# Performance work log

Measured on AMD Instinct MI355X. Metric: run time of the kernel, lower is better.

## Reference

```python
import jax, jax.numpy as jnp
import numpy as np

D_MODEL = 1024
NUM_HEADS = 16
D_K = D_MODEL // NUM_HEADS
B, S = 2, 2048


def setup_inputs() -> dict:
    key = jax.random.key(0)
    ks = jax.random.split(key, 6)
    scale = 1.0 / np.sqrt(D_MODEL)
    x = jax.random.normal(ks[0], (B, S, D_MODEL), dtype=jnp.float32)
    # causal mask: 1 where masked (future positions), per masked_fill(mask == 1, -inf)
    mask = jnp.triu(jnp.ones((S, S), dtype=jnp.int32), k=1)
    Wq = jax.random.normal(ks[1], (D_MODEL, D_MODEL), dtype=jnp.float32) * scale
    Wk = jax.random.normal(ks[2], (D_MODEL, D_MODEL), dtype=jnp.float32) * scale
    Wv = jax.random.normal(ks[3], (D_MODEL, D_MODEL), dtype=jnp.float32) * scale
    Wo = jax.random.normal(ks[4], (D_MODEL, D_MODEL), dtype=jnp.float32) * scale
    zeros = jnp.zeros((D_MODEL,), dtype=jnp.float32)
    return {"x": x, "mask": mask, "Wq": Wq, "bq": zeros, "Wk": Wk, "bk": zeros,
            "Wv": Wv, "bv": zeros, "Wo": Wo, "bo": zeros}


def reference(x, mask, Wq, bq, Wk, bk, Wv, bv, Wo, bo):
    b, s, d = x.shape
    # linear projections (torch nn.Linear: x @ W^T + b; here W stored as [in, out])
    Q = x @ Wq + bq
    K = x @ Wk + bk
    V = x @ Wv + bv
    # split heads -> (b, h, s, d_k)
    def split(t):
        return t.reshape(b, s, NUM_HEADS, D_K).transpose(0, 2, 1, 3)
    Q, K, V = split(Q), split(K), split(V)
    scale = 1.0 / jnp.sqrt(jnp.float32(D_K))
    scores = jnp.einsum("bhqd,bhkd->bhqk", Q, K) * scale  # (b,h,s,s)
    scores = jnp.where(mask[None, None, :, :] == 1, -jnp.inf, scores)
    attn = jax.nn.softmax(scores, axis=-1)
    out = jnp.einsum("bhqk,bhkd->bhqd", attn, V)
    out = out.transpose(0, 2, 1, 3).reshape(b, s, d)  # concat heads
    return out @ Wo + bo
```

## Files before the change

### kernel.cpp

```cpp
#include <hip/hip_runtime.h>
#include <hip/hip_bf16.h>
#include <cstdint>
#include <cmath>

#define DM 1024
#define NH 16
#define DK 64
#define NB 2
#define SS 2048
#define MM (NB*SS)

typedef unsigned short u16;
typedef uint32_t u32;
typedef __attribute__((ext_vector_type(4))) float f32x4;
typedef __attribute__((ext_vector_type(8))) short s16x8;
typedef __attribute__((ext_vector_type(2))) uint32_t u32x2;

__device__ __forceinline__ u16 f2bf(float f) {
    __hip_bfloat16 h = __float2bfloat16(f);
    return __builtin_bit_cast(u16, h);
}
__device__ __forceinline__ float bf2f(u16 u) {
    u32 x = (u32)u << 16;
    return __builtin_bit_cast(float, x);
}

__device__ __forceinline__ u32 cvtpk(float a, float b) {
    u32 r;
    asm("v_cvt_pk_bf16_f32 %0, %1, %2" : "=v"(r) : "v"(a), "v"(b));
    return r;
}

__device__ __forceinline__ void gload_lds16(void* lds, const void* g) {
    __builtin_amdgcn_global_load_lds(
        (const __attribute__((address_space(1))) uint32_t*)g,
        (__attribute__((address_space(3))) uint32_t*)lds, 16, 0, 0);
}

__device__ __forceinline__ int swz(int row, int cb) {
    return row * 128 + ((((cb) >> 4) ^ (row & 7)) << 4) + ((cb) & 15);
}

__global__ void mha_prep(const float* __restrict__ x, u16* __restrict__ xb,
                         const float* __restrict__ W0, const float* __restrict__ W1,
                         const float* __restrict__ W2, const float* __restrict__ W3,
                         u16* __restrict__ WtBase) {
    const int bid = blockIdx.x, tid = threadIdx.x;
    if (bid < 4096) {
        int i = (bid * 256 + tid) * 4;
        float4 v = *reinterpret_cast<const float4*>(x + i);
        ushort4 o;
        o.x = f2bf(v.x); o.y = f2bf(v.y); o.z = f2bf(v.z); o.w = f2bf(v.w);
        *reinterpret_cast<ushort4*>(xb + i) = o;
        return;
    }
    __shared__ float t[32][33];
    const int b2 = bid - 4096;
    const int mat = b2 >> 10, rem = b2 & 1023;
    const int cx = rem & 31, cy = rem >> 5;
    const float* W = (mat == 0) ? W0 : (mat == 1) ? W1 : (mat == 2) ? W2 : W3;
    u16* Wt = WtBase + (size_t)mat * DM * DM;
    const int c0 = cx * 32, r0 = cy * 32;
    const int tx = tid & 31, ty = tid >> 5;
#pragma unroll
    for (int i = ty; i < 32; i += 8)
        t[i][tx] = W[(size_t)(r0 + i) * DM + c0 + tx];
    __syncthreads();
#pragma unroll
    for (int i = ty; i < 32; i += 8)
        Wt[(size_t)(c0 + i) * DM + r0 + tx] = f2bf(t[tx][i]);
}

__device__ __forceinline__ void gemm_loop_db(const u16* __restrict__ A, const u16* __restrict__ Bt,
                                             int m0, int n0, char* smem , f32x4 acc[4][4]) {
    const int tid = threadIdx.x;
    const int wave = tid >> 6, lane = tid & 63;
    const int lr = lane & 15, kg = lane >> 4;
    const int wr = wave >> 1, wc = wave & 1;

    auto STAGE = [&](int buf, int k0) {
        char* As = smem + buf * 32768;
        char* Bs = As + 16384;
#pragma unroll
        for (int i = 0; i < 4; ++i) {
            const int o   = ((wave * 4 + i) * 64 + lane) * 16;
            const int row = o >> 7;
            const int kb  = o & 127;
            gload_lds16(As + o, A  + (size_t)(m0 + row) * DM + k0 + (kb >> 1));
            gload_lds16(Bs + o, Bt + (size_t)(n0 + row) * DM + k0 + (kb >> 1));
        }
    };

    STAGE(0, 0);
    for (int t = 0; t < 16; ++t) {
        if (t + 1 < 16) {
            STAGE((t + 1) & 1, (t + 1) * 64);
            asm volatile("s_waitcnt vmcnt(8)" ::: "memory");
        } else {
            asm volatile("s_waitcnt vmcnt(0)" ::: "memory");
        }
        __builtin_amdgcn_sched_barrier(0);
        __builtin_amdgcn_s_barrier();
        __builtin_amdgcn_sched_barrier(0);

        const u16 (*As)[64] = reinterpret_cast<const u16(*)[64]>(smem + (t & 1) * 32768);
        const u16 (*Bs)[64] = reinterpret_cast<const u16(*)[64]>(smem + (t & 1) * 32768 + 16384);
#pragma unroll
        for (int kk = 0; kk < 64; kk += 32) {
            s16x8 a[4], b[4];
#pragma unroll
            for (int m = 0; m < 4; ++m)
                a[m] = *reinterpret_cast<const s16x8*>(&As[wr * 64 + m * 16 + lr][kk + kg * 8]);
#pragma unroll
            for (int n = 0; n < 4; ++n)
                b[n] = *reinterpret_cast<const s16x8*>(&Bs[wc * 64 + n * 16 + lr][kk + kg * 8]);
#pragma unroll
            for (int m = 0; m < 4; ++m)
#pragma unroll
                for (int n = 0; n < 4; ++n)
                    acc[m][n] = __builtin_amdgcn_mfma_f32_16x16x32_bf16(a[m], b[n], acc[m][n], 0, 0, 0);
        }
        __builtin_amdgcn_sched_barrier(0);
        __builtin_amdgcn_s_barrier();
        __builtin_amdgcn_sched_barrier(0);
    }
}

__global__ __launch_bounds__(256, 2) void mha_gemm_qkv(const u16* __restrict__ xb, const u16* __restrict__ Wt,
                                                       const float* __restrict__ bq, const float* __restrict__ bk,
                                                       const float* __restrict__ bv, u16* __restrict__ qkv) {
    __shared__ __align__(16) char smem[65536];
    const int m0 = blockIdx.x * 128, n0 = blockIdx.y * 128;
    const int z = blockIdx.z;
    const float* bias = (z == 0) ? bq : (z == 1) ? bk : bv;
    const float scale = (z == 0) ? 0.125f * 1.44269504088896f : 1.0f;
    u16* Cout = qkv + (size_t)z * MM * DM;

    f32x4 acc[4][4] = {};
    gemm_loop_db(xb, Wt + (size_t)z * DM * DM, m0, n0, smem, acc);

    const int tid = threadIdx.x;
    const int wave = tid >> 6, lane = tid & 63;
    const int lr = lane & 15, kg = lane >> 4;
    const int wr = wave >> 1, wc = wave & 1;

#pragma unroll
    for (int m = 0; m < 4; ++m)
#pragma unroll
        for (int n = 0; n < 4; ++n) {
            const int col = wc * 64 + n * 16 + lr;
            const float bv2 = bias[n0 + col];
#pragma unroll
            for (int j2 = 0; j2 < 4; ++j2) {
                const int row = wr * 64 + m * 16 + kg * 4 + j2;
                const float v = (acc[m][n][j2] + bv2) * scale;
                int imgoff;
                if (z == 0) {
                    imgoff = row * 256 + (col >> 6) * 128 + (col & 63) * 2;
                } else if (z == 1) {
                    imgoff = ((row >> 6) * 2 + (col >> 6)) * 8192 + swz(row & 63, (col & 63) * 2);
                } else {
                    imgoff = ((row >> 6) * 2 + (col >> 6)) * 8192
                           + swz(col & 63, ((row & 63) >> 1) * 4 + (row & 1) * 2);
                }
                *reinterpret_cast<u16*>(smem + imgoff) = f2bf(v);
            }
        }
    __syncthreads();
    const int bb = m0 >> 11, s0 = m0 & (SS - 1);
    const int kt0 = s0 >> 6, h0 = n0 >> 6;
#pragma unroll
    for (int it = 0; it < 8; ++it) {
        const int c = it * 256 + tid;
        const s16x8 v = *reinterpret_cast<const s16x8*>(smem + c * 16);
        u16* dst;
        if (z == 0) {
            const int srow = c >> 4, inrow = c & 15;
            const int hl = inrow >> 3, d0 = (inrow & 7) * 8;
            dst = Cout + (((size_t)(bb * NH + h0 + hl) * SS + (s0 + srow)) * DK) + d0;
        } else {
            const int quad = c >> 9, off = (c & 511) * 8;
            const int ktl = quad >> 1, hl = quad & 1;
            dst = Cout + ((size_t)(bb * NH + h0 + hl) * 32 + kt0 + ktl) * 4096 + off;
        }
        *reinterpret_cast<s16x8*>(dst) = v;
    }
}

__global__ __launch_bounds__(256, 2) void mha_gemm_out(const u16* __restrict__ AO, const u16* __restrict__ WoT,
                                                       const float* __restrict__ bo, float* __restrict__ out) {
    __shared__ __align__(16) char smem[65536];
    const int m0 = blockIdx.x * 128, n0 = blockIdx.y * 128;

    f32x4 acc[4][4] = {};
    gemm_loop_db(AO, WoT, m0, n0, smem, acc);

    const int tid = threadIdx.x;
    const int wave = tid >> 6, lane = tid & 63;
    const int lr = lane & 15, kg = lane >> 4;
    const int wr = wave >> 1, wc = wave & 1;
#pragma unroll
    for (int m = 0; m < 4; ++m)
#pragma unroll
        for (int n = 0; n < 4; ++n) {
            const int col = n0 + wc * 64 + n * 16 + lr;
            const float bv = bo[col];
#pragma unroll
            for (int j2 = 0; j2 < 4; ++j2) {
                const int row = m0 + wr * 64 + m * 16 + kg * 4 + j2;
                out[(size_t)row * DM + col] = acc[m][n][j2] + bv;
            }
        }
}

__device__ const unsigned char JQT[48] = {
    15,31,30,31, 14,29,30,28,29, 13,27,28,26,27, 12,25,26,24,25,
    11,23,24,22,23, 10,21,22,20,21, 9,19,20,18,19, 8,17,18,16,17,
    7,16, 6,5,4,3,2,1,0};
__device__ const unsigned char JKS[48] = {
    0,0,15,16, 0,0,0,14,15, 0,0,0,13,14, 0,0,0,12,13,
    0,0,0,11,12, 0,0,0,10,11, 0,0,0,9,10, 0,0,0,8,9,
    0,0, 0,0,0,0,0,0,0};
__device__ const unsigned char JKL[48] = {
    16,16,16,16, 15,15,15,15,15, 14,14,14,14,14, 13,13,13,13,13,
    12,12,12,12,12, 11,11,11,11,11, 10,10,10,10,10, 9,9,9,9,9,
    8,8, 7,6,5,4,3,2,1};
__device__ const unsigned char JSL[48] = {
    255,30,29,31, 255,26,28,25,27, 255,22,24,21,23, 255,18,20,17,19,
    255,14,16,13,15, 255,10,12,9,11, 255,6,8,5,7, 255,2,4,1,3,
    255,0, 255,255,255,255,255,255,255};

__global__ __launch_bounds__(256, 4) void mha_attn(const u16* __restrict__ Qb, const u16* __restrict__ Kswz,
                                                   const u16* __restrict__ Vtswz, u16* __restrict__ AO,
                                                   u16* __restrict__ Opart, float* __restrict__ lpart) {
    __shared__ __align__(16) char lds[40960];

    const int bid = blockIdx.x;
    const int bh  = bid & 31;
    const int job = bid >> 5;
    const int qt   = JQT[job];
    const int kst  = JKS[job];
    const int klen = JKL[job];
    const int slot = JSL[job];
    const int qb = qt * 64;

    const int tid = threadIdx.x, w = tid >> 6, lane = tid & 63;
    const int lr = lane & 15, kg = lane >> 4;

    const u16* Qh = Qb + (size_t)bh * SS * DK;
    const char* Ktiles = (const char*)(Kswz  + (size_t)bh * 32 * 4096);
    const char* Vtiles = (const char*)(Vtswz + (size_t)bh * 32 * 4096);
    const int bb = bh >> 4, hh = bh & (NH - 1);
    char* psb = lds + 32768 + w * 2048;
    const int o = tid * 16;

    const int qrow = qb + w * 16 + lr;
    const s16x8 qf0 = *reinterpret_cast<const s16x8*>(Qh + (size_t)qrow * DK + kg * 8);
    const s16x8 qf1 = *reinterpret_cast<const s16x8*>(Qh + (size_t)qrow * DK + 32 + kg * 8);
    f32x4 accO[4] = {};
    float lp = 0.f;

    const int kend = kst + klen;
    {
        const char* Kt = Ktiles + kst * 8192;
        const char* Vt = Vtiles + kst * 8192;
        gload_lds16(lds + o,                 Kt + o);
        gload_lds16(lds + o + 4096,          Kt + o + 4096);
        gload_lds16(lds + 16384 + o,         Vt + o);
        gload_lds16(lds + 16384 + o + 4096,  Vt + o + 4096);
    }

    for (int t = kst; t < kend; ++t) {
        const int buf = (t - kst) & 1;
        asm volatile("s_waitcnt vmcnt(0)" ::: "memory");
        __syncthreads();
        if (t + 1 < kend) {
            const char* Kt = Ktiles + (t + 1) * 8192;
            const char* Vt = Vtiles + (t + 1) * 8192;
            char* kb2 = lds + (buf ^ 1) * 8192;
            char* vb2 = lds + 16384 + (buf ^ 1) * 8192;
            gload_lds16(kb2 + o,        Kt + o);
            gload_lds16(kb2 + o + 4096, Kt + o + 4096);
            gload_lds16(vb2 + o,        Vt + o);
            gload_lds16(vb2 + o + 4096, Vt + o + 4096);
        }
        const char* ksb = lds + buf * 8192;
        const char* vtb = lds + 16384 + buf * 8192;

        f32x4 sc[4];
#pragma unroll
        for (int f = 0; f < 4; ++f) {
            s16x8 kf0 = *reinterpret_cast<const s16x8*>(ksb + swz(f * 16 + lr, kg * 16));
            s16x8 kf1 = *reinterpret_cast<const s16x8*>(ksb + swz(f * 16 + lr, 64 + kg * 16));
            f32x4 s = {};
            s = __builtin_amdgcn_mfma_f32_16x16x32_bf16(kf0, qf0, s, 0, 0, 0);
            s = __builtin_amdgcn_mfma_f32_16x16x32_bf16(kf1, qf1, s, 0, 0, 0);
            sc[f] = s;
        }
#pragma unroll
        for (int f = 0; f < 4; ++f)
#pragma unroll
            for (int j = 0; j < 4; ++j)
                sc[f][j] = __builtin_amdgcn_exp2f(sc[f][j]);
        if (t == qt) {
            const int qloc = w * 16 + lr;
#pragma unroll
            for (int f = 0; f < 4; ++f) {
                const int kc = f * 16 + kg * 4;
#pragma unroll
                for (int j = 0; j < 4; ++j)
                    if (kc + j > qloc) sc[f][j] = 0.f;
            }
        }
        float fs0 = 0.f, fs1 = 0.f;
#pragma unroll
        for (int f = 0; f < 4; ++f) {
            u32x2 pp;
            pp[0] = cvtpk(sc[f][0], sc[f][1]);
            pp[1] = cvtpk(sc[f][2], sc[f][3]);
            *reinterpret_cast<u32x2*>(psb + swz(lr, f * 32 + kg * 8)) = pp;
            const float s01 = sc[f][0] + sc[f][1], s23 = sc[f][2] + sc[f][3];
            if (f & 1) fs1 += s01 + s23; else fs0 += s01 + s23;
        }
        lp += fs0 + fs1;

        const s16x8 pf0 = *reinterpret_cast<const s16x8*>(psb + swz(lr, kg * 16));
        const s16x8 pf1 = *reinterpret_cast<const s16x8*>(psb + swz(lr, 64 + kg * 16));
#pragma unroll
        for (int db = 0; db < 4; ++db) {
            s16x8 vf0 = *reinterpret_cast<const s16x8*>(vtb + swz(db * 16 + lr, kg * 16));
            s16x8 vf1 = *reinterpret_cast<const s16x8*>(vtb + swz(db * 16 + lr, 64 + kg * 16));
            accO[db] = __builtin_amdgcn_mfma_f32_16x16x32_bf16(pf0, vf0, accO[db], 0, 0, 0);
            accO[db] = __builtin_amdgcn_mfma_f32_16x16x32_bf16(pf1, vf1, accO[db], 0, 0, 0);
        }
    }

    lp += __shfl_xor(lp, 16, 64);
    lp += __shfl_xor(lp, 32, 64);

    if (slot == 255) {
        float inv[4];
#pragma unroll
        for (int j = 0; j < 4; ++j)
            inv[j] = 1.0f / __shfl(lp, kg * 4 + j, 64);
#pragma unroll
        for (int db = 0; db < 4; ++db) {
            const int d = db * 16 + lr;
#pragma unroll
            for (int j = 0; j < 4; ++j) {
                const int s = qb + w * 16 + kg * 4 + j;
                AO[((size_t)(bb * SS + s)) * DM + hh * DK + d] = f2bf(accO[db][j] * inv[j]);
            }
        }
    } else {
        const int idx = bh * 32 + slot;
        u16* Od = Opart + (size_t)idx * 4096;
#pragma unroll
        for (int db = 0; db < 4; ++db) {
            const int d = db * 16 + lr;
#pragma unroll
            for (int j = 0; j < 4; ++j)
                Od[(w * 16 + kg * 4 + j) * 64 + d] = f2bf(accO[db][j]);
        }
        if (lane < 16)
            lpart[idx * 64 + w * 16 + lane] = lp;
    }
}

__global__ __launch_bounds__(256) void mha_combine(const u16* __restrict__ Opart,
                                                   const float* __restrict__ lpart,
                                                   u16* __restrict__ AO) {
    const int blk = blockIdx.x;
    const int bh = blk & 31, q = blk >> 5;
    const int qt = 16 + q;
    const int t = threadIdx.x;
    const int row = t >> 2, c0 = (t & 3) * 16;
    const int idx0 = bh * 32 + q * 2;
    const u16* O0 = Opart + (size_t)idx0 * 4096 + row * 64 + c0;
    const u16* O1 = O0 + 4096;
    const float l = lpart[idx0 * 64 + row] + lpart[(idx0 + 1) * 64 + row];
    const float inv = 1.0f / l;
    const int bb = bh >> 4, hh = bh & (NH - 1);
    const int s = qt * 64 + row;
    u16* dst = AO + ((size_t)(bb * SS + s)) * DM + hh * DK + c0;
#pragma unroll
    for (int h = 0; h < 2; ++h) {
        s16x8 a = *reinterpret_cast<const s16x8*>(O0 + h * 8);
        s16x8 b = *reinterpret_cast<const s16x8*>(O1 + h * 8);
        u16* ap = (u16*)&a; u16* bp = (u16*)&b;
        u16 ov[8];
#pragma unroll
        for (int i = 0; i < 8; ++i)
            ov[i] = f2bf((bf2f(ap[i]) + bf2f(bp[i])) * inv);
        *reinterpret_cast<ushort4*>(dst + h * 8) = *reinterpret_cast<ushort4*>(&ov[0]);
        *reinterpret_cast<ushort4*>(dst + h * 8 + 4) = *reinterpret_cast<ushort4*>(&ov[4]);
    }
}

extern "C" void kernel_launch(void* const* d_in, const int* in_sizes, int n_in,
                              void* d_out, int out_size, void* d_ws, size_t ws_size,
                              hipStream_t stream) {
    const float* x  = (const float*)d_in[0];
    const float* Wq = (const float*)d_in[2];
    const float* bq = (const float*)d_in[3];
    const float* Wk = (const float*)d_in[4];
    const float* bk = (const float*)d_in[5];
    const float* Wv = (const float*)d_in[6];
    const float* bv = (const float*)d_in[7];
    const float* Wo = (const float*)d_in[8];
    const float* bo = (const float*)d_in[9];
    float* out = (float*)d_out;

    char* ws = (char*)d_ws;
    u16* xb  = (u16*)(ws);
    u16* Wt  = (u16*)(ws + ((size_t)8  << 20));
    u16* qkv = (u16*)(ws + ((size_t)16 << 20));
    u16* AO  = (u16*)(ws + ((size_t)40 << 20));
    u16*   Opart = (u16*)(ws);
    float* lpart = (float*)(ws + ((size_t)8 << 20));

    mha_prep<<<dim3(8192), dim3(256), 0, stream>>>(x, xb, Wq, Wk, Wv, Wo, Wt);
    mha_gemm_qkv<<<dim3(32, 8, 3), dim3(256), 0, stream>>>(xb, Wt, bq, bk, bv, qkv);
    mha_attn<<<dim3(1536), dim3(256), 0, stream>>>(qkv, qkv + (size_t)4194304, qkv + (size_t)8388608,
                                                   AO, Opart, lpart);
    mha_combine<<<dim3(512), dim3(256), 0, stream>>>(Opart, lpart, AO);
    mha_gemm_out<<<dim3(32, 8), dim3(256), 0, stream>>>(AO, Wt + (size_t)3 * DM * DM, bo, out);
}
```

Baseline: 107.3 us.

## Rewrite QKV projection GEMM with 256x256 tiles, 8 waves, and phased prefetch

Replaces the 128x128, 4-wave QKV GEMM with a 256x256 tile computed by 8 waves (512 threads). The K loop is split into four quadrant phases, each issuing the next half-tile prefetch into a swizzled LDS double buffer ahead of its MFMAs, and MFMA blocks run at raised wave priority. The goal is more operand reuse per byte loaded and better overlap of loads with compute. The grid shrinks to 192 blocks, under one wave of blocks on a 256-CU part. The epilogue now writes scattered 2-byte global stores instead of staging through LDS for 16-byte coalesced writes, which may cost store bandwidth.

```diff
diff --git a/kernel.cpp b/kernel.cpp
--- a/kernel.cpp
+++ b/kernel.cpp
@@ -40,6 +40,10 @@
 __device__ __forceinline__ int swz(int row, int cb) {
     return row * 128 + ((((cb) >> 4) ^ (row & 7)) << 4) + ((cb) & 15);
 }
+
+#define FENCE_BAR  do { __builtin_amdgcn_sched_barrier(0); \
+                        __builtin_amdgcn_s_barrier();      \
+                        __builtin_amdgcn_sched_barrier(0); } while (0)
 
 __global__ void mha_prep(const float* __restrict__ x, u16* __restrict__ xb,
                          const float* __restrict__ W0, const float* __restrict__ W1,
@@ -71,6 +75,120 @@
         Wt[(size_t)(c0 + i) * DM + r0 + tx] = f2bf(t[tx][i]);
 }
 
+template<int QA, int QB>
+__device__ __forceinline__ void phase8(const char* smem, int cur,
+                                       int wm, int wn, int lr, int kg,
+                                       f32x4 (&acc)[8][4]) {
+    const char* Ab = smem + cur * 32768 + QA * 16384;
+    const char* Bb = smem + 65536 + cur * 32768 + QB * 16384;
+    s16x8 af[4][2], bf[2][2];
+#pragma unroll
+    for (int m = 0; m < 4; ++m)
+#pragma unroll
+        for (int ks = 0; ks < 2; ++ks)
+            af[m][ks] = *reinterpret_cast<const s16x8*>(Ab + swz(wm * 64 + m * 16 + lr, ks * 64 + kg * 16));
+#pragma unroll
+    for (int n = 0; n < 2; ++n)
+#pragma unroll
+        for (int ks = 0; ks < 2; ++ks)
+            bf[n][ks] = *reinterpret_cast<const s16x8*>(Bb + swz(wn * 32 + n * 16 + lr, ks * 64 + kg * 16));
+    __builtin_amdgcn_s_setprio(1);
+#pragma unroll
+    for (int m = 0; m < 4; ++m)
+#pragma unroll
+        for (int n = 0; n < 2; ++n)
+#pragma unroll
+            for (int ks = 0; ks < 2; ++ks)
+                acc[QA * 4 + m][QB * 2 + n] =
+                    __builtin_amdgcn_mfma_f32_16x16x32_bf16(af[m][ks], bf[n][ks],
+                                                            acc[QA * 4 + m][QB * 2 + n], 0, 0, 0);
+    __builtin_amdgcn_s_setprio(0);
+}
+
+__global__ __launch_bounds__(512, 2) void mha_gemm_qkv(const u16* __restrict__ xb, const u16* __restrict__ Wt,
+                                                       const float* __restrict__ bq, const float* __restrict__ bk,
+                                                       const float* __restrict__ bv, u16* __restrict__ qkv) {
+    __shared__ __align__(16) char smem[131072];
+    const int bid = blockIdx.x;
+    const int mtile = bid & 15, ntile = bid >> 4;
+    const int m0 = mtile * 256, n0g = ntile * 256;
+    const int z = n0g >> 10;
+    const int n0loc = n0g & 1023;
+    const u16* At  = xb + (size_t)m0 * DM;
+    const u16* Btm = Wt + (size_t)z * DM * DM + (size_t)n0loc * DM;
+    const float* bias = (z == 0) ? bq : (z == 1) ? bk : bv;
+    const float scale = (z == 0) ? 0.125f * 1.44269504088896f : 1.0f;
+    u16* Cout = qkv + (size_t)z * MM * DM;
+
+    const int tid = threadIdx.x, lane = tid & 63, wid = tid >> 6;
+    const int lr = lane & 15, kg = lane >> 4;
+    const int wm = wid >> 2, wn = wid & 3;
+    f32x4 acc[8][4] = {};
+
+    auto STAGE = [&](int isB, int half, int buf, int kt) {
+        char* base = smem + (isB ? 65536 : 0) + buf * 32768 + half * 16384;
+        const u16* src = isB ? Btm : At;
+#pragma unroll
+        for (int i = 0; i < 2; ++i) {
+            const int o = tid * 16 + i * 8192;
+            const int r = o >> 7, slot = (o >> 4) & 7;
+            gload_lds16(base + o,
+                        src + (size_t)(half * 128 + r) * DM + kt * 64 + ((slot ^ (r & 7)) << 3));
+        }
+    };
+
+    STAGE(0, 0, 0, 0); STAGE(1, 0, 0, 0); STAGE(0, 1, 0, 0); STAGE(1, 1, 0, 0);
+
+    for (int t = 0; t < 16; ++t) {
+        const int cur = t & 1, nxt = cur ^ 1;
+        const bool pf = (t + 1 < 16);
+        asm volatile("s_waitcnt vmcnt(4)" ::: "memory");
+        FENCE_BAR;
+        if (pf) STAGE(0, 0, nxt, t + 1);
+        phase8<0, 0>(smem, cur, wm, wn, lr, kg, acc);
+        if (pf) asm volatile("s_waitcnt vmcnt(4)" ::: "memory");
+        else    asm volatile("s_waitcnt vmcnt(2)" ::: "memory");
+        FENCE_BAR;
+        if (pf) STAGE(1, 0, nxt, t + 1);
+        phase8<1, 0>(smem, cur, wm, wn, lr, kg, acc);
+        if (pf) asm volatile("s_waitcnt vmcnt(4)" ::: "memory");
+        else    asm volatile("s_waitcnt vmcnt(0)" ::: "memory");
+        FENCE_BAR;
+        if (pf) STAGE(0, 1, nxt, t + 1);
+        phase8<1, 1>(smem, cur, wm, wn, lr, kg, acc);
+        if (pf) STAGE(1, 1, nxt, t + 1);
+        phase8<0, 1>(smem, cur, wm, wn, lr, kg, acc);
+    }
+
+#pragma unroll
+    for (int qa = 0; qa < 2; ++qa)
+#pragma unroll
+        for (int m = 0; m < 4; ++m)
+#pragma unroll
+            for (int qb = 0; qb < 2; ++qb)
+#pragma unroll
+                for (int n = 0; n < 2; ++n) {
+                    const int colg = n0loc + qb * 128 + wn * 32 + n * 16 + lr;
+                    const int h = colg >> 6, d = colg & 63;
+                    const float bv2 = bias[colg];
+#pragma unroll
+                    for (int j = 0; j < 4; ++j) {
+                        const int srow = m0 + qa * 128 + wm * 64 + m * 16 + kg * 4 + j;
+                        const int bb = srow >> 11, s = srow & (SS - 1);
+                        const float v = (acc[qa * 4 + m][qb * 2 + n][j] + bv2) * scale;
+                        if (z == 0) {
+                            Cout[(((size_t)(bb * NH + h) * SS + s) * DK) + d] = f2bf(v);
+                        } else {
+                            const int kt = s >> 6, r = s & 63;
+                            const size_t tb = ((size_t)(bb * NH + h) * 32 + kt) * 4096;
+                            const int bo = (z == 1) ? swz(r, d * 2)
+                                                    : swz(d, (r >> 1) * 4 + (r & 1) * 2);
+                            Cout[tb + (bo >> 1)] = f2bf(v);
+                        }
+                    }
+                }
+}
+
 __device__ __forceinline__ void gemm_loop_db(const u16* __restrict__ A, const u16* __restrict__ Bt,
                                              int m0, int n0, char* smem , f32x4 acc[4][4]) {
     const int tid = threadIdx.x;
@@ -99,10 +217,7 @@
         } else {
             asm volatile("s_waitcnt vmcnt(0)" ::: "memory");
         }
-        __builtin_amdgcn_sched_barrier(0);
-        __builtin_amdgcn_s_barrier();
-        __builtin_amdgcn_sched_barrier(0);
-
+        FENCE_BAR;
         const u16 (*As)[64] = reinterpret_cast<const u16(*)[64]>(smem + (t & 1) * 32768);
         const u16 (*Bs)[64] = reinterpret_cast<const u16(*)[64]>(smem + (t & 1) * 32768 + 16384);
 #pragma unroll
@@ -120,70 +235,7 @@
                 for (int n = 0; n < 4; ++n)
                     acc[m][n] = __builtin_amdgcn_mfma_f32_16x16x32_bf16(a[m], b[n], acc[m][n], 0, 0, 0);
         }
-        __builtin_amdgcn_sched_barrier(0);
-        __builtin_amdgcn_s_barrier();
-        __builtin_amdgcn_sched_barrier(0);
-    }
-}
-
-__global__ __launch_bounds__(256, 2) void mha_gemm_qkv(const u16* __restrict__ xb, const u16* __restrict__ Wt,
-                                                       const float* __restrict__ bq, const float* __restrict__ bk,
-                                                       const float* __restrict__ bv, u16* __restrict__ qkv) {
-    __shared__ __align__(16) char smem[65536];
-    const int m0 = blockIdx.x * 128, n0 = blockIdx.y * 128;
-    const int z = blockIdx.z;
-    const float* bias = (z == 0) ? bq : (z == 1) ? bk : bv;
-    const float scale = (z == 0) ? 0.125f * 1.44269504088896f : 1.0f;
-    u16* Cout = qkv + (size_t)z * MM * DM;
-
-    f32x4 acc[4][4] = {};
-    gemm_loop_db(xb, Wt + (size_t)z * DM * DM, m0, n0, smem, acc);
-
-    const int tid = threadIdx.x;
-    const int wave = tid >> 6, lane = tid & 63;
-    const int lr = lane & 15, kg = lane >> 4;
-    const int wr = wave >> 1, wc = wave & 1;
-
-#pragma unroll
-    for (int m = 0; m < 4; ++m)
-#pragma unroll
-        for (int n = 0; n < 4; ++n) {
-            const int col = wc * 64 + n * 16 + lr;
-            const float bv2 = bias[n0 + col];
-#pragma unroll
-            for (int j2 = 0; j2 < 4; ++j2) {
-                const int row = wr * 64 + m * 16 + kg * 4 + j2;
-                const float v = (acc[m][n][j2] + bv2) * scale;
-                int imgoff;
-                if (z == 0) {
-                    imgoff = row * 256 + (col >> 6) * 128 + (col & 63) * 2;
-                } else if (z == 1) {
-                    imgoff = ((row >> 6) * 2 + (col >> 6)) * 8192 + swz(row & 63, (col & 63) * 2);
-                } else {
-                    imgoff = ((row >> 6) * 2 + (col >> 6)) * 8192
-                           + swz(col & 63, ((row & 63) >> 1) * 4 + (row & 1) * 2);
-                }
-                *reinterpret_cast<u16*>(smem + imgoff) = f2bf(v);
-            }
-        }
-    __syncthreads();
-    const int bb = m0 >> 11, s0 = m0 & (SS - 1);
-    const int kt0 = s0 >> 6, h0 = n0 >> 6;
-#pragma unroll
-    for (int it = 0; it < 8; ++it) {
-        const int c = it * 256 + tid;
-        const s16x8 v = *reinterpret_cast<const s16x8*>(smem + c * 16);
-        u16* dst;
-        if (z == 0) {
-            const int srow = c >> 4, inrow = c & 15;
-            const int hl = inrow >> 3, d0 = (inrow & 7) * 8;
-            dst = Cout + (((size_t)(bb * NH + h0 + hl) * SS + (s0 + srow)) * DK) + d0;
-        } else {
-            const int quad = c >> 9, off = (c & 511) * 8;
-            const int ktl = quad >> 1, hl = quad & 1;
-            dst = Cout + ((size_t)(bb * NH + h0 + hl) * 32 + kt0 + ktl) * 4096 + off;
-        }
-        *reinterpret_cast<s16x8*>(dst) = v;
+        FENCE_BAR;
     }
 }
 
@@ -420,7 +472,7 @@
     float* lpart = (float*)(ws + ((size_t)8 << 20));
 
     mha_prep<<<dim3(8192), dim3(256), 0, stream>>>(x, xb, Wq, Wk, Wv, Wo, Wt);
-    mha_gemm_qkv<<<dim3(32, 8, 3), dim3(256), 0, stream>>>(xb, Wt, bq, bk, bv, qkv);
+    mha_gemm_qkv<<<dim3(192), dim3(512), 0, stream>>>(xb, Wt, bq, bk, bv, qkv);
     mha_attn<<<dim3(1536), dim3(256), 0, stream>>>(qkv, qkv + (size_t)4194304, qkv + (size_t)8388608,
                                                    AO, Opart, lpart);
     mha_combine<<<dim3(512), dim3(256), 0, stream>>>(Opart, lpart, AO);
```

Result: no change. 109.2 us (+1.8%).

## Remap QKV GEMM blocks per XCD and use single-buffered LDS loop

Applied to the files above, without the earlier changes.

The QKV projection GEMM now launches as a 1D grid. Its block index is remapped so each group of blocks sharing a low index (one XCD under round-robin dispatch) works on a fixed set of four row tiles across all column tiles and Q/K/V, which should improve L2 reuse of the activation tiles. Its K loop also drops the double-buffered async LDS pipeline for a simpler single-buffer loop with __syncthreads, halving LDS per block to 32KB so more blocks can fit. The cost is that global loads no longer overlap with MFMA work inside a block, so any gain depends on the added occupancy and locality hiding that latency.

```diff
diff --git a/kernel.cpp b/kernel.cpp
--- a/kernel.cpp
+++ b/kernel.cpp
@@ -40,6 +40,10 @@
 __device__ __forceinline__ int swz(int row, int cb) {
     return row * 128 + ((((cb) >> 4) ^ (row & 7)) << 4) + ((cb) & 15);
 }
+
+#define FENCE_BAR  do { __builtin_amdgcn_sched_barrier(0); \
+                        __builtin_amdgcn_s_barrier();      \
+                        __builtin_amdgcn_sched_barrier(0); } while (0)
 
 __global__ void mha_prep(const float* __restrict__ x, u16* __restrict__ xb,
                          const float* __restrict__ W0, const float* __restrict__ W1,
@@ -71,40 +75,25 @@
         Wt[(size_t)(c0 + i) * DM + r0 + tx] = f2bf(t[tx][i]);
 }
 
-__device__ __forceinline__ void gemm_loop_db(const u16* __restrict__ A, const u16* __restrict__ Bt,
-                                             int m0, int n0, char* smem , f32x4 acc[4][4]) {
+__device__ __forceinline__ void gemm_loop(const u16* __restrict__ A, const u16* __restrict__ Bt,
+                                          int m0, int n0,
+                                          u16 (*As)[64], u16 (*Bs)[64], f32x4 acc[4][4]) {
     const int tid = threadIdx.x;
     const int wave = tid >> 6, lane = tid & 63;
     const int lr = lane & 15, kg = lane >> 4;
     const int wr = wave >> 1, wc = wave & 1;
 
-    auto STAGE = [&](int buf, int k0) {
-        char* As = smem + buf * 32768;
-        char* Bs = As + 16384;
+    for (int k0 = 0; k0 < DM; k0 += 64) {
+        __syncthreads();
 #pragma unroll
         for (int i = 0; i < 4; ++i) {
             const int o   = ((wave * 4 + i) * 64 + lane) * 16;
             const int row = o >> 7;
             const int kb  = o & 127;
-            gload_lds16(As + o, A  + (size_t)(m0 + row) * DM + k0 + (kb >> 1));
-            gload_lds16(Bs + o, Bt + (size_t)(n0 + row) * DM + k0 + (kb >> 1));
-        }
-    };
-
-    STAGE(0, 0);
-    for (int t = 0; t < 16; ++t) {
-        if (t + 1 < 16) {
-            STAGE((t + 1) & 1, (t + 1) * 64);
-            asm volatile("s_waitcnt vmcnt(8)" ::: "memory");
-        } else {
-            asm volatile("s_waitcnt vmcnt(0)" ::: "memory");
-        }
-        __builtin_amdgcn_sched_barrier(0);
-        __builtin_amdgcn_s_barrier();
-        __builtin_amdgcn_sched_barrier(0);
-
-        const u16 (*As)[64] = reinterpret_cast<const u16(*)[64]>(smem + (t & 1) * 32768);
-        const u16 (*Bs)[64] = reinterpret_cast<const u16(*)[64]>(smem + (t & 1) * 32768 + 16384);
+            gload_lds16((char*)As + o, A  + (size_t)(m0 + row) * DM + k0 + (kb >> 1));
+            gload_lds16((char*)Bs + o, Bt + (size_t)(n0 + row) * DM + k0 + (kb >> 1));
+        }
+        __syncthreads();
 #pragma unroll
         for (int kk = 0; kk < 64; kk += 32) {
             s16x8 a[4], b[4];
@@ -120,30 +109,36 @@
                 for (int n = 0; n < 4; ++n)
                     acc[m][n] = __builtin_amdgcn_mfma_f32_16x16x32_bf16(a[m], b[n], acc[m][n], 0, 0, 0);
         }
-        __builtin_amdgcn_sched_barrier(0);
-        __builtin_amdgcn_s_barrier();
-        __builtin_amdgcn_sched_barrier(0);
     }
 }
 
 __global__ __launch_bounds__(256, 2) void mha_gemm_qkv(const u16* __restrict__ xb, const u16* __restrict__ Wt,
                                                        const float* __restrict__ bq, const float* __restrict__ bk,
                                                        const float* __restrict__ bv, u16* __restrict__ qkv) {
-    __shared__ __align__(16) char smem[65536];
-    const int m0 = blockIdx.x * 128, n0 = blockIdx.y * 128;
-    const int z = blockIdx.z;
+    __shared__ __align__(16) char smem[32768];
+    u16 (*As)[64] = reinterpret_cast<u16(*)[64]>(smem);
+    u16 (*Bs)[64] = reinterpret_cast<u16(*)[64]>(smem + 16384);
+
+    const int bid = blockIdx.x;
+    const int j = bid & 7, r = bid >> 3;
+    const int bx = j * 4 + (r & 3);
+    const int by = (r >> 2) & 7;
+    const int z  = r >> 5;
+    const int m0 = bx * 128, n0 = by * 128;
+
     const float* bias = (z == 0) ? bq : (z == 1) ? bk : bv;
     const float scale = (z == 0) ? 0.125f * 1.44269504088896f : 1.0f;
     u16* Cout = qkv + (size_t)z * MM * DM;
 
     f32x4 acc[4][4] = {};
-    gemm_loop_db(xb, Wt + (size_t)z * DM * DM, m0, n0, smem, acc);
+    gemm_loop(xb, Wt + (size_t)z * DM * DM, m0, n0, As, Bs, acc);
 
     const int tid = threadIdx.x;
     const int wave = tid >> 6, lane = tid & 63;
     const int lr = lane & 15, kg = lane >> 4;
     const int wr = wave >> 1, wc = wave & 1;
 
+    __syncthreads();
 #pragma unroll
     for (int m = 0; m < 4; ++m)
 #pragma unroll
@@ -184,6 +179,56 @@
             dst = Cout + ((size_t)(bb * NH + h0 + hl) * 32 + kt0 + ktl) * 4096 + off;
         }
         *reinterpret_cast<s16x8*>(dst) = v;
+    }
+}
+
+__device__ __forceinline__ void gemm_loop_db(const u16* __restrict__ A, const u16* __restrict__ Bt,
+                                             int m0, int n0, char* smem , f32x4 acc[4][4]) {
+    const int tid = threadIdx.x;
+    const int wave = tid >> 6, lane = tid & 63;
+    const int lr = lane & 15, kg = lane >> 4;
+    const int wr = wave >> 1, wc = wave & 1;
+
+    auto STAGE = [&](int buf, int k0) {
+        char* As = smem + buf * 32768;
+        char* Bs = As + 16384;
+#pragma unroll
+        for (int i = 0; i < 4; ++i) {
+            const int o   = ((wave * 4 + i) * 64 + lane) * 16;
+            const int row = o >> 7;
+            const int kb  = o & 127;
+            gload_lds16(As + o, A  + (size_t)(m0 + row) * DM + k0 + (kb >> 1));
+            gload_lds16(Bs + o, Bt + (size_t)(n0 + row) * DM + k0 + (kb >> 1));
+        }
+    };
+
+    STAGE(0, 0);
+    for (int t = 0; t < 16; ++t) {
+        if (t + 1 < 16) {
+            STAGE((t + 1) & 1, (t + 1) * 64);
+            asm volatile("s_waitcnt vmcnt(8)" ::: "memory");
+        } else {
+            asm volatile("s_waitcnt vmcnt(0)" ::: "memory");
+        }
+        FENCE_BAR;
+        const u16 (*As)[64] = reinterpret_cast<const u16(*)[64]>(smem + (t & 1) * 32768);
+        const u16 (*Bs)[64] = reinterpret_cast<const u16(*)[64]>(smem + (t & 1) * 32768 + 16384);
+#pragma unroll
+        for (int kk = 0; kk < 64; kk += 32) {
+            s16x8 a[4], b[4];
+#pragma unroll
+            for (int m = 0; m < 4; ++m)
+                a[m] = *reinterpret_cast<const s16x8*>(&As[wr * 64 + m * 16 + lr][kk + kg * 8]);
+#pragma unroll
+            for (int n = 0; n < 4; ++n)
+                b[n] = *reinterpret_cast<const s16x8*>(&Bs[wc * 64 + n * 16 + lr][kk + kg * 8]);
+#pragma unroll
+            for (int m = 0; m < 4; ++m)
+#pragma unroll
+                for (int n = 0; n < 4; ++n)
+                    acc[m][n] = __builtin_amdgcn_mfma_f32_16x16x32_bf16(a[m], b[n], acc[m][n], 0, 0, 0);
+        }
+        FENCE_BAR;
     }
 }
 
@@ -390,7 +435,7 @@
         u16* ap = (u16*)&a; u16* bp = (u16*)&b;
         u16 ov[8];
 #pragma unroll
-        for (int i = 0; i < 8; ++i)
+    for (int i = 0; i < 8; ++i)
             ov[i] = f2bf((bf2f(ap[i]) + bf2f(bp[i])) * inv);
         *reinterpret_cast<ushort4*>(dst + h * 8) = *reinterpret_cast<ushort4*>(&ov[0]);
         *reinterpret_cast<ushort4*>(dst + h * 8 + 4) = *reinterpret_cast<ushort4*>(&ov[4]);
@@ -420,7 +465,7 @@
     float* lpart = (float*)(ws + ((size_t)8 << 20));
 
     mha_prep<<<dim3(8192), dim3(256), 0, stream>>>(x, xb, Wq, Wk, Wv, Wo, Wt);
-    mha_gemm_qkv<<<dim3(32, 8, 3), dim3(256), 0, stream>>>(xb, Wt, bq, bk, bv, qkv);
+    mha_gemm_qkv<<<dim3(768), dim3(256), 0, stream>>>(xb, Wt, bq, bk, bv, qkv);
     mha_attn<<<dim3(1536), dim3(256), 0, stream>>>(qkv, qkv + (size_t)4194304, qkv + (size_t)8388608,
                                                    AO, Opart, lpart);
     mha_combine<<<dim3(512), dim3(256), 0, stream>>>(Opart, lpart, AO);
```

After: 103.5 us. -3.5%, faster.
